# Performance work log

Hardware: AMD Instinct MI355X
Metric: run time of the kernel (lower is better)

Reference implementation:

```python
import jax, jax.numpy as jnp
import numpy as np

D_MODEL = 512
NHEAD = 8
HEAD_DIM = D_MODEL // NHEAD
WINDOW = 128


def setup_inputs() -> dict:
    key = jax.random.key(0)
    ks = jax.random.split(key, 5)
    B, S = 2, 2048
    scale = D_MODEL ** -0.5
    return {
        "x": jax.random.normal(ks[0], (B, S, D_MODEL), dtype=jnp.float32),
        # weights stored [in, out] so y = x @ W (equivalent to nn.Linear, bias=False)
        "Wq": jax.random.normal(ks[1], (D_MODEL, D_MODEL), dtype=jnp.float32) * scale,
        "Wk": jax.random.normal(ks[2], (D_MODEL, D_MODEL), dtype=jnp.float32) * scale,
        "Wv": jax.random.normal(ks[3], (D_MODEL, D_MODEL), dtype=jnp.float32) * scale,
        "Wo": jax.random.normal(ks[4], (D_MODEL, D_MODEL), dtype=jnp.float32) * scale,
    }


def reference(x, Wq, Wk, Wv, Wo):
    B, S, _ = x.shape
    # projections -> [B, H, S, D]
    def split_heads(y):
        return y.reshape(B, S, NHEAD, HEAD_DIM).transpose(0, 2, 1, 3)
    q = split_heads(x @ Wq)
    k = split_heads(x @ Wk)
    v = split_heads(x @ Wv)

    # causal sliding window: position p attends to [p - WINDOW + 1, p]
    pos = jnp.arange(S)
    offs = jnp.arange(WINDOW)
    idx = pos[:, None] - (WINDOW - 1) + offs[None, :]          # [S, W]
    valid = idx >= 0                                            # mask out-of-range (padded) slots
    idxc = jnp.clip(idx, 0, S - 1)

    k_w = k[:, :, idxc]                                         # [B, H, S, W, D]
    v_w = v[:, :, idxc]                                         # [B, H, S, W, D]

    inv_sqrt_d = jnp.float32(1.0 / np.sqrt(HEAD_DIM))
    scores = jnp.einsum('bhsd,bhswd->bhsw', q, k_w) * inv_sqrt_d
    scores = jnp.where(valid[None, None], scores, -jnp.inf)    # same as torch -inf masking of pads
    attn = jax.nn.softmax(scores, axis=-1)                      # last slot (self) always valid
    out = jnp.einsum('bhsw,bhswd->bhsd', attn, v_w)             # [B, H, S, D]
    out = out.transpose(0, 2, 1, 3).reshape(B, S, D_MODEL)
    return out @ Wo
```

## Files before the change

kernel.cpp:

```cpp
#include <hip/hip_runtime.h>

typedef __attribute__((ext_vector_type(8))) short bf16x8;
typedef __attribute__((ext_vector_type(4))) float f32x4;

#define D_MODEL 512
#define SEQ 2048
#define NB 2
#define NHEAD 8
#define HDIM 64
#define WIN 128

__device__ inline unsigned short f2bf(float f) {
    unsigned u = __float_as_uint(f);
    unsigned r = (u + 0x7fffu + ((u >> 16) & 1u)) >> 16;
    return (unsigned short)r;
}

__device__ inline void async_load16(const void* g, void* l) {
    __builtin_amdgcn_global_load_lds((const __attribute__((address_space(1))) void*)g,
                                     (__attribute__((address_space(3))) void*)l, 16, 0, 0);
}

__global__ __launch_bounds__(256) void conv_x(const float* __restrict__ x,
                                              unsigned short* __restrict__ xc) {
    int i = blockIdx.x * 256 + threadIdx.x;
    float4 v = ((const float4*)x)[i];
    ushort4 o;
    o.x = f2bf(v.x); o.y = f2bf(v.y); o.z = f2bf(v.z); o.w = f2bf(v.w);
    ((ushort4*)xc)[i] = o;
}

__global__ __launch_bounds__(256) void zero_out(float4* __restrict__ p) {
    p[blockIdx.x * 256 + threadIdx.x] = (float4){0.f, 0.f, 0.f, 0.f};
}

__global__ __launch_bounds__(256) void conv_wt(const float* __restrict__ Wq,
                                               const float* __restrict__ Wk,
                                               const float* __restrict__ Wv,
                                               const float* __restrict__ Wo,
                                               unsigned short* __restrict__ Wt) {
    __shared__ float tile[32 * 33];
    const int mat = blockIdx.z;
    const float* W = mat == 0 ? Wq : mat == 1 ? Wk : mat == 2 ? Wv : Wo;
    const int ti = blockIdx.x, tj = blockIdx.y;
    const int t = threadIdx.x;
    {
        int c = t & 31, r4 = (t >> 5) * 4;
        #pragma unroll
        for (int e = 0; e < 4; e++)
            tile[(r4 + e) * 33 + c] = W[(size_t)(ti * 32 + r4 + e) * 512 + tj * 32 + c];
    }
    __syncthreads();
    {
        int rr = t & 31, c4 = (t >> 5) * 4;
        #pragma unroll
        for (int e = 0; e < 4; e++)
            Wt[(size_t)mat * 262144 + (size_t)(tj * 32 + c4 + e) * 512 + ti * 32 + rr] =
                f2bf(tile[rr * 33 + c4 + e]);
    }
}

__device__ inline void storeC(float* C, size_t i, float v) { C[i] = v; }
__device__ inline void storeC(unsigned short* C, size_t i, float v) { C[i] = f2bf(v); }

template <typename OUT, bool ATOMIC>
__global__ __launch_bounds__(256) void gemm_bt(const unsigned short* __restrict__ A,
                                               const unsigned short* __restrict__ Bt,
                                               OUT* __restrict__ C, int Nstride,
                                               int kPerSplit) {
    __shared__ unsigned short As[128 * 32];
    __shared__ unsigned short Bs[128 * 32];
    const int t = threadIdx.x;
    const int w = t >> 6, l = t & 63;
    const int mBase = blockIdx.x * 128;
    const int nBase = blockIdx.y * 128;
    const int kBase = blockIdx.z * kPerSplit;
    const int r0 = t >> 2, koff = (t & 3) * 8;
    const unsigned short* a0 = A + (size_t)(mBase + r0) * 512 + koff;
    const unsigned short* a1 = A + (size_t)(mBase + 64 + r0) * 512 + koff;
    const unsigned short* b0 = Bt + (size_t)(nBase + r0) * 512 + koff;
    const unsigned short* b1 = Bt + (size_t)(nBase + 64 + r0) * 512 + koff;
    unsigned short* asd0 = &As[t * 8];
    unsigned short* asd1 = &As[2048 + t * 8];
    unsigned short* bsd0 = &Bs[t * 8];
    unsigned short* bsd1 = &Bs[2048 + t * 8];

    const int lane_m = l & 15;
    const int kg = (l >> 4) * 8;
    const int wr = (w >> 1) * 64, wc = (w & 1) * 64;

    f32x4 acc[4][4];
    #pragma unroll
    for (int i = 0; i < 4; i++)
        #pragma unroll
        for (int j = 0; j < 4; j++) acc[i][j] = (f32x4){0.f, 0.f, 0.f, 0.f};

    for (int k0 = kBase; k0 < kBase + kPerSplit; k0 += 32) {
        async_load16(a0 + k0, asd0);
        async_load16(a1 + k0, asd1);
        async_load16(b0 + k0, bsd0);
        async_load16(b1 + k0, bsd1);
        __syncthreads();
        bf16x8 af[4], bfr[4];
        #pragma unroll
        for (int i = 0; i < 4; i++)
            af[i] = *(const bf16x8*)&As[(wr + i * 16 + lane_m) * 32 + kg];
        #pragma unroll
        for (int j = 0; j < 4; j++)
            bfr[j] = *(const bf16x8*)&Bs[(wc + j * 16 + lane_m) * 32 + kg];
        #pragma unroll
        for (int i = 0; i < 4; i++)
            #pragma unroll
            for (int j = 0; j < 4; j++)
                acc[i][j] = __builtin_amdgcn_mfma_f32_16x16x32_bf16(af[i], bfr[j], acc[i][j], 0, 0, 0);
        __syncthreads();
    }
    const int rRow = (l >> 4) * 4;
    const int cCol = l & 15;
    #pragma unroll
    for (int i = 0; i < 4; i++)
        #pragma unroll
        for (int j = 0; j < 4; j++)
            #pragma unroll
            for (int r = 0; r < 4; r++) {
                size_t row = (size_t)(mBase + wr + i * 16 + rRow + r);
                size_t col = (size_t)(nBase + wc + j * 16 + cCol);
                if (ATOMIC)
                    unsafeAtomicAdd((float*)&C[row * (size_t)Nstride + col], acc[i][j][r]);
                else
                    storeC(C, row * (size_t)Nstride + col, acc[i][j][r]);
            }
}

__global__ __launch_bounds__(256) void transpose_v(const unsigned short* __restrict__ QKV,
                                                   unsigned short* __restrict__ Vtg) {
    __shared__ unsigned short tile[64 * 72];
    const int t = threadIdx.x;
    const int s0 = blockIdx.x * 64, h = blockIdx.y, b = blockIdx.z;
    const unsigned short* base = QKV + (size_t)b * SEQ * 1536 + 1024 + h * 64;
    for (int i = t; i < 64 * 8; i += 256) {
        int r = i >> 3, c8 = i & 7;
        *(uint4*)&tile[r * 72 + c8 * 8] = *(const uint4*)(base + (size_t)(s0 + r) * 1536 + c8 * 8);
    }
    __syncthreads();
    for (int i = t; i < 64 * 8; i += 256) {
        int d = i >> 3, c8 = i & 7;
        unsigned short tmp[8];
        #pragma unroll
        for (int e = 0; e < 8; e++) tmp[e] = tile[(c8 * 8 + e) * 72 + d];
        uint4 ov;
        ov.x = (unsigned)tmp[0] | ((unsigned)tmp[1] << 16);
        ov.y = (unsigned)tmp[2] | ((unsigned)tmp[3] << 16);
        ov.z = (unsigned)tmp[4] | ((unsigned)tmp[5] << 16);
        ov.w = (unsigned)tmp[6] | ((unsigned)tmp[7] << 16);
        *(uint4*)(Vtg + ((size_t)(b * 8 + h) * 64 + d) * SEQ + s0 + c8 * 8) = ov;
    }
}

__global__ __launch_bounds__(256) void attn_mfma(const unsigned short* __restrict__ QKV,
                                                 const unsigned short* __restrict__ Vtg,
                                                 unsigned short* __restrict__ AO) {
    __shared__ unsigned short Ks[192 * 72];
    __shared__ unsigned short Qs[64 * 72];
    __shared__ unsigned short Vs[64 * 200];
    __shared__ unsigned short Pb[4][16 * 40];

    const int t = threadIdx.x;
    const int w = t >> 6, l = t & 63;
    const int s0 = blockIdx.x * 64;
    const int h = blockIdx.y, b = blockIdx.z;
    const unsigned short* base = QKV + (size_t)b * SEQ * 1536;

    for (int i = t; i < 192 * 8; i += 256) {
        int j = i >> 3, c8 = i & 7;
        int g = s0 - 127 + j;
        g = g < 0 ? 0 : (g > SEQ - 1 ? SEQ - 1 : g);
        *(uint4*)&Ks[j * 72 + c8 * 8] =
            *(const uint4*)(base + (size_t)g * 1536 + 512 + h * 64 + c8 * 8);
    }
    for (int i = t; i < 64 * 8; i += 256) {
        int r = i >> 3, c8 = i & 7;
        *(uint4*)&Qs[r * 72 + c8 * 8] =
            *(const uint4*)(base + (size_t)(s0 + r) * 1536 + h * 64 + c8 * 8);
    }
    const unsigned short* vrow0 = Vtg + ((size_t)(b * 8 + h) * 64) * SEQ + (s0 - 127);
    for (int i = t; i < 64 * 24; i += 256) {
        int d = i / 24, c = i % 24;
        *(uint4*)&Vs[d * 200 + c * 8] = *(const uint4*)(vrow0 + (size_t)d * SEQ + c * 8);
    }
    __syncthreads();

    const int lm = l & 15, lk = (l >> 4) * 8;

    f32x4 sc[12];
    #pragma unroll
    for (int kb = 0; kb < 12; kb++) sc[kb] = (f32x4){0.f, 0.f, 0.f, 0.f};
    bf16x8 aq[2];
    #pragma unroll
    for (int ks = 0; ks < 2; ks++)
        aq[ks] = *(const bf16x8*)&Qs[(w * 16 + lm) * 72 + ks * 32 + lk];
    #pragma unroll
    for (int kb = 0; kb < 12; kb++) {
        #pragma unroll
        for (int ks = 0; ks < 2; ks++) {
            bf16x8 bk = *(const bf16x8*)&Ks[(kb * 16 + lm) * 72 + ks * 32 + lk];
            sc[kb] = __builtin_amdgcn_mfma_f32_16x16x32_bf16(aq[ks], bk, sc[kb], 0, 0, 0);
        }
    }

    const int qr0 = (l >> 4) * 4;
    const int jlo_g = 127 - s0;
    float mrow[4] = {-1e30f, -1e30f, -1e30f, -1e30f};
    #pragma unroll
    for (int kb = 0; kb < 12; kb++) {
        int j = kb * 16 + lm;
        #pragma unroll
        for (int r = 0; r < 4; r++) {
            int qi = w * 16 + qr0 + r;
            bool valid = (j >= qi) & (j <= qi + 127) & (j >= jlo_g);
            float v = valid ? sc[kb][r] * 0.125f : -1e30f;
            sc[kb][r] = v;
            mrow[r] = fmaxf(mrow[r], v);
        }
    }
    #pragma unroll
    for (int r = 0; r < 4; r++) {
        mrow[r] = fmaxf(mrow[r], __shfl_xor(mrow[r], 1));
        mrow[r] = fmaxf(mrow[r], __shfl_xor(mrow[r], 2));
        mrow[r] = fmaxf(mrow[r], __shfl_xor(mrow[r], 4));
        mrow[r] = fmaxf(mrow[r], __shfl_xor(mrow[r], 8));
    }
    float srow[4] = {0.f, 0.f, 0.f, 0.f};
    #pragma unroll
    for (int kb = 0; kb < 12; kb++)
        #pragma unroll
        for (int r = 0; r < 4; r++) {
            float p = __expf(sc[kb][r] - mrow[r]);
            sc[kb][r] = p;
            srow[r] += p;
        }
    #pragma unroll
    for (int r = 0; r < 4; r++) {
        srow[r] += __shfl_xor(srow[r], 1);
        srow[r] += __shfl_xor(srow[r], 2);
        srow[r] += __shfl_xor(srow[r], 4);
        srow[r] += __shfl_xor(srow[r], 8);
        srow[r] = 1.f / srow[r];
    }

    f32x4 ov[4];
    #pragma unroll
    for (int nb = 0; nb < 4; nb++) ov[nb] = (f32x4){0.f, 0.f, 0.f, 0.f};
    unsigned short* pb = &Pb[w][0];
    #pragma unroll
    for (int c = 0; c < 6; c++) {
        #pragma unroll
        for (int kk = 0; kk < 2; kk++)
            #pragma unroll
            for (int r = 0; r < 4; r++)
                pb[(qr0 + r) * 40 + kk * 16 + lm] = f2bf(sc[2 * c + kk][r]);
        bf16x8 ap = *(const bf16x8*)&pb[lm * 40 + lk];
        #pragma unroll
        for (int nb = 0; nb < 4; nb++) {
            bf16x8 bv = *(const bf16x8*)&Vs[(nb * 16 + lm) * 200 + c * 32 + lk];
            ov[nb] = __builtin_amdgcn_mfma_f32_16x16x32_bf16(ap, bv, ov[nb], 0, 0, 0);
        }
    }

    #pragma unroll
    for (int nb = 0; nb < 4; nb++)
        #pragma unroll
        for (int r = 0; r < 4; r++) {
            size_t row = (size_t)(b * SEQ + s0 + w * 16 + qr0 + r);
            AO[row * 512 + h * 64 + nb * 16 + lm] = f2bf(ov[nb][r] * srow[r]);
        }
}

extern "C" void kernel_launch(void* const* d_in, const int* in_sizes, int n_in,
                              void* d_out, int out_size, void* d_ws, size_t ws_size,
                              hipStream_t stream) {
    const float* x  = (const float*)d_in[0];
    const float* Wq = (const float*)d_in[1];
    const float* Wk = (const float*)d_in[2];
    const float* Wv = (const float*)d_in[3];
    const float* Wo = (const float*)d_in[4];
    float* out = (float*)d_out;

    char* ws = (char*)d_ws;
    unsigned short* xc  = (unsigned short*)ws;
    unsigned short* Wt  = (unsigned short*)(ws + 4u * 1024 * 1024);
    unsigned short* QKV = (unsigned short*)(ws + 6u * 1024 * 1024);
    unsigned short* AO  = (unsigned short*)(ws + 18u * 1024 * 1024);
    unsigned short* Vtg = (unsigned short*)(ws + 22u * 1024 * 1024 + 2048);

    conv_x<<<2048, 256, 0, stream>>>(x, xc);
    conv_wt<<<dim3(16, 16, 4), 256, 0, stream>>>(Wq, Wk, Wv, Wo, Wt);
    zero_out<<<2048, 256, 0, stream>>>((float4*)out);
    gemm_bt<unsigned short, false><<<dim3(32, 12, 1), 256, 0, stream>>>(xc, Wt, QKV, 1536, 512);
    transpose_v<<<dim3(32, 8, 2), 256, 0, stream>>>(QKV, Vtg);
    attn_mfma<<<dim3(32, 8, 2), 256, 0, stream>>>(QKV, Vtg, AO);
    gemm_bt<float, true><<<dim3(32, 4, 2), 256, 0, stream>>>(AO, Wt + 3 * 262144, out, 512, 256);
}
```

Baseline: 124.4 us.

## Cut launch count: merge prep kernels, fold V transpose into attention, drop split-K atomics

Merges the x and weight conversion kernels into one launch, removes the zero-fill and separate V-transpose kernels, and has the attention kernel transpose V into LDS itself using an XOR-swizzled layout. Both GEMMs now use 64-row tiles with full K per block and plain stores, so the output projection no longer needs atomics or a zeroed output. The aim is to cut launch overhead and extra global traffic on a launch-bound pipeline. In exchange, the GEMMs reuse less data per tile, and the scalar LDS transpose stores in attention may cause bank conflicts.

```diff
diff --git a/kernel.cpp b/kernel.cpp
--- a/kernel.cpp
+++ b/kernel.cpp
@@ -5,9 +5,7 @@
 
 #define D_MODEL 512
 #define SEQ 2048
-#define NB 2
 #define NHEAD 8
-#define HDIM 64
 #define WIN 128
 
 __device__ inline unsigned short f2bf(float f) {
@@ -21,29 +19,28 @@
                                      (__attribute__((address_space(3))) void*)l, 16, 0, 0);
 }
 
-__global__ __launch_bounds__(256) void conv_x(const float* __restrict__ x,
-                                              unsigned short* __restrict__ xc) {
-    int i = blockIdx.x * 256 + threadIdx.x;
-    float4 v = ((const float4*)x)[i];
-    ushort4 o;
-    o.x = f2bf(v.x); o.y = f2bf(v.y); o.z = f2bf(v.z); o.w = f2bf(v.w);
-    ((ushort4*)xc)[i] = o;
-}
-
-__global__ __launch_bounds__(256) void zero_out(float4* __restrict__ p) {
-    p[blockIdx.x * 256 + threadIdx.x] = (float4){0.f, 0.f, 0.f, 0.f};
-}
-
-__global__ __launch_bounds__(256) void conv_wt(const float* __restrict__ Wq,
-                                               const float* __restrict__ Wk,
-                                               const float* __restrict__ Wv,
-                                               const float* __restrict__ Wo,
-                                               unsigned short* __restrict__ Wt) {
+__global__ __launch_bounds__(256) void prep(const float* __restrict__ x,
+                                            const float* __restrict__ Wq,
+                                            const float* __restrict__ Wk,
+                                            const float* __restrict__ Wv,
+                                            const float* __restrict__ Wo,
+                                            unsigned short* __restrict__ xc,
+                                            unsigned short* __restrict__ Wt) {
     __shared__ float tile[32 * 33];
-    const int mat = blockIdx.z;
+    const int t = threadIdx.x;
+    if (blockIdx.x < 2048) {
+        int i = blockIdx.x * 256 + t;
+        float4 v = ((const float4*)x)[i];
+        ushort4 o;
+        o.x = f2bf(v.x); o.y = f2bf(v.y); o.z = f2bf(v.z); o.w = f2bf(v.w);
+        ((ushort4*)xc)[i] = o;
+        return;
+    }
+    int idx = blockIdx.x - 2048;
+    const int mat = idx >> 8;
+    const int rem = idx & 255;
+    const int ti = rem & 15, tj = rem >> 4;
     const float* W = mat == 0 ? Wq : mat == 1 ? Wk : mat == 2 ? Wv : Wo;
-    const int ti = blockIdx.x, tj = blockIdx.y;
-    const int t = threadIdx.x;
     {
         int c = t & 31, r4 = (t >> 5) * 4;
         #pragma unroll
@@ -63,102 +60,57 @@
 __device__ inline void storeC(float* C, size_t i, float v) { C[i] = v; }
 __device__ inline void storeC(unsigned short* C, size_t i, float v) { C[i] = f2bf(v); }
 
-template <typename OUT, bool ATOMIC>
-__global__ __launch_bounds__(256) void gemm_bt(const unsigned short* __restrict__ A,
-                                               const unsigned short* __restrict__ Bt,
-                                               OUT* __restrict__ C, int Nstride,
-                                               int kPerSplit) {
-    __shared__ unsigned short As[128 * 32];
-    __shared__ unsigned short Bs[128 * 32];
+template <typename OUT, int NT>
+__global__ __launch_bounds__(256) void gemm64(const unsigned short* __restrict__ A,
+                                              const unsigned short* __restrict__ Bt,
+                                              OUT* __restrict__ C, int Nstride) {
+    __shared__ unsigned short As[64 * 32];
+    __shared__ unsigned short Bs[NT * 16 * 32];
     const int t = threadIdx.x;
     const int w = t >> 6, l = t & 63;
-    const int mBase = blockIdx.x * 128;
-    const int nBase = blockIdx.y * 128;
-    const int kBase = blockIdx.z * kPerSplit;
+    const int mBase = blockIdx.x * 64;
+    const int nBase = blockIdx.y * (NT * 16);
     const int r0 = t >> 2, koff = (t & 3) * 8;
     const unsigned short* a0 = A + (size_t)(mBase + r0) * 512 + koff;
-    const unsigned short* a1 = A + (size_t)(mBase + 64 + r0) * 512 + koff;
     const unsigned short* b0 = Bt + (size_t)(nBase + r0) * 512 + koff;
     const unsigned short* b1 = Bt + (size_t)(nBase + 64 + r0) * 512 + koff;
-    unsigned short* asd0 = &As[t * 8];
-    unsigned short* asd1 = &As[2048 + t * 8];
+    unsigned short* asd  = &As[t * 8];
     unsigned short* bsd0 = &Bs[t * 8];
     unsigned short* bsd1 = &Bs[2048 + t * 8];
 
-    const int lane_m = l & 15;
+    const int lm = l & 15;
     const int kg = (l >> 4) * 8;
-    const int wr = (w >> 1) * 64, wc = (w & 1) * 64;
-
-    f32x4 acc[4][4];
-    #pragma unroll
-    for (int i = 0; i < 4; i++)
-        #pragma unroll
-        for (int j = 0; j < 4; j++) acc[i][j] = (f32x4){0.f, 0.f, 0.f, 0.f};
-
-    for (int k0 = kBase; k0 < kBase + kPerSplit; k0 += 32) {
-        async_load16(a0 + k0, asd0);
-        async_load16(a1 + k0, asd1);
+
+    f32x4 acc[NT];
+    #pragma unroll
+    for (int j = 0; j < NT; j++) acc[j] = (f32x4){0.f, 0.f, 0.f, 0.f};
+
+    for (int k0 = 0; k0 < 512; k0 += 32) {
+        async_load16(a0 + k0, asd);
         async_load16(b0 + k0, bsd0);
-        async_load16(b1 + k0, bsd1);
+        if (NT == 8) async_load16(b1 + k0, bsd1);
         __syncthreads();
-        bf16x8 af[4], bfr[4];
-        #pragma unroll
-        for (int i = 0; i < 4; i++)
-            af[i] = *(const bf16x8*)&As[(wr + i * 16 + lane_m) * 32 + kg];
-        #pragma unroll
-        for (int j = 0; j < 4; j++)
-            bfr[j] = *(const bf16x8*)&Bs[(wc + j * 16 + lane_m) * 32 + kg];
-        #pragma unroll
-        for (int i = 0; i < 4; i++)
-            #pragma unroll
-            for (int j = 0; j < 4; j++)
-                acc[i][j] = __builtin_amdgcn_mfma_f32_16x16x32_bf16(af[i], bfr[j], acc[i][j], 0, 0, 0);
+        bf16x8 af = *(const bf16x8*)&As[(w * 16 + lm) * 32 + kg];
+        #pragma unroll
+        for (int j = 0; j < NT; j++) {
+            bf16x8 bfr = *(const bf16x8*)&Bs[(j * 16 + lm) * 32 + kg];
+            acc[j] = __builtin_amdgcn_mfma_f32_16x16x32_bf16(af, bfr, acc[j], 0, 0, 0);
+        }
         __syncthreads();
     }
     const int rRow = (l >> 4) * 4;
     const int cCol = l & 15;
     #pragma unroll
-    for (int i = 0; i < 4; i++)
-        #pragma unroll
-        for (int j = 0; j < 4; j++)
-            #pragma unroll
-            for (int r = 0; r < 4; r++) {
-                size_t row = (size_t)(mBase + wr + i * 16 + rRow + r);
-                size_t col = (size_t)(nBase + wc + j * 16 + cCol);
-                if (ATOMIC)
-                    unsafeAtomicAdd((float*)&C[row * (size_t)Nstride + col], acc[i][j][r]);
-                else
-                    storeC(C, row * (size_t)Nstride + col, acc[i][j][r]);
-            }
-}
-
-__global__ __launch_bounds__(256) void transpose_v(const unsigned short* __restrict__ QKV,
-                                                   unsigned short* __restrict__ Vtg) {
-    __shared__ unsigned short tile[64 * 72];
-    const int t = threadIdx.x;
-    const int s0 = blockIdx.x * 64, h = blockIdx.y, b = blockIdx.z;
-    const unsigned short* base = QKV + (size_t)b * SEQ * 1536 + 1024 + h * 64;
-    for (int i = t; i < 64 * 8; i += 256) {
-        int r = i >> 3, c8 = i & 7;
-        *(uint4*)&tile[r * 72 + c8 * 8] = *(const uint4*)(base + (size_t)(s0 + r) * 1536 + c8 * 8);
-    }
-    __syncthreads();
-    for (int i = t; i < 64 * 8; i += 256) {
-        int d = i >> 3, c8 = i & 7;
-        unsigned short tmp[8];
-        #pragma unroll
-        for (int e = 0; e < 8; e++) tmp[e] = tile[(c8 * 8 + e) * 72 + d];
-        uint4 ov;
-        ov.x = (unsigned)tmp[0] | ((unsigned)tmp[1] << 16);
-        ov.y = (unsigned)tmp[2] | ((unsigned)tmp[3] << 16);
-        ov.z = (unsigned)tmp[4] | ((unsigned)tmp[5] << 16);
-        ov.w = (unsigned)tmp[6] | ((unsigned)tmp[7] << 16);
-        *(uint4*)(Vtg + ((size_t)(b * 8 + h) * 64 + d) * SEQ + s0 + c8 * 8) = ov;
-    }
+    for (int j = 0; j < NT; j++)
+        #pragma unroll
+        for (int r = 0; r < 4; r++) {
+            size_t row = (size_t)(mBase + w * 16 + rRow + r);
+            size_t col = (size_t)(nBase + j * 16 + cCol);
+            storeC(C, row * (size_t)Nstride + col, acc[j][r]);
+        }
 }
 
 __global__ __launch_bounds__(256) void attn_mfma(const unsigned short* __restrict__ QKV,
-                                                 const unsigned short* __restrict__ Vtg,
                                                  unsigned short* __restrict__ AO) {
     __shared__ unsigned short Ks[192 * 72];
     __shared__ unsigned short Qs[64 * 72];
@@ -183,10 +135,18 @@
         *(uint4*)&Qs[r * 72 + c8 * 8] =
             *(const uint4*)(base + (size_t)(s0 + r) * 1536 + h * 64 + c8 * 8);
     }
-    const unsigned short* vrow0 = Vtg + ((size_t)(b * 8 + h) * 64) * SEQ + (s0 - 127);
-    for (int i = t; i < 64 * 24; i += 256) {
-        int d = i / 24, c = i % 24;
-        *(uint4*)&Vs[d * 200 + c * 8] = *(const uint4*)(vrow0 + (size_t)d * SEQ + c * 8);
+    for (int i = t; i < 192 * 8; i += 256) {
+        int j = i >> 3, c8 = i & 7;
+        int g = s0 - 127 + j;
+        g = g < 0 ? 0 : (g > SEQ - 1 ? SEQ - 1 : g);
+        uint4 vv = *(const uint4*)(base + (size_t)g * 1536 + 1024 + h * 64 + c8 * 8);
+        unsigned short e16[8];
+        *(uint4*)e16 = vv;
+        int chunk = (j >> 3) ^ c8;
+        int off = chunk * 8 + (j & 7);
+        #pragma unroll
+        for (int e = 0; e < 8; e++)
+            Vs[(c8 * 8 + e) * 200 + off] = e16[e];
     }
     __syncthreads();
 
@@ -262,7 +222,10 @@
         bf16x8 ap = *(const bf16x8*)&pb[lm * 40 + lk];
         #pragma unroll
         for (int nb = 0; nb < 4; nb++) {
-            bf16x8 bv = *(const bf16x8*)&Vs[(nb * 16 + lm) * 200 + c * 32 + lk];
+            int d = nb * 16 + lm;
+            int cj = c * 4 + (l >> 4);
+            int off = ((cj ^ ((d >> 3) & 7)) * 8);
+            bf16x8 bv = *(const bf16x8*)&Vs[d * 200 + off];
             ov[nb] = __builtin_amdgcn_mfma_f32_16x16x32_bf16(ap, bv, ov[nb], 0, 0, 0);
         }
     }
@@ -291,13 +254,9 @@
     unsigned short* Wt  = (unsigned short*)(ws + 4u * 1024 * 1024);
     unsigned short* QKV = (unsigned short*)(ws + 6u * 1024 * 1024);
     unsigned short* AO  = (unsigned short*)(ws + 18u * 1024 * 1024);
-    unsigned short* Vtg = (unsigned short*)(ws + 22u * 1024 * 1024 + 2048);
-
-    conv_x<<<2048, 256, 0, stream>>>(x, xc);
-    conv_wt<<<dim3(16, 16, 4), 256, 0, stream>>>(Wq, Wk, Wv, Wo, Wt);
-    zero_out<<<2048, 256, 0, stream>>>((float4*)out);
-    gemm_bt<unsigned short, false><<<dim3(32, 12, 1), 256, 0, stream>>>(xc, Wt, QKV, 1536, 512);
-    transpose_v<<<dim3(32, 8, 2), 256, 0, stream>>>(QKV, Vtg);
-    attn_mfma<<<dim3(32, 8, 2), 256, 0, stream>>>(QKV, Vtg, AO);
-    gemm_bt<float, true><<<dim3(32, 4, 2), 256, 0, stream>>>(AO, Wt + 3 * 262144, out, 512, 256);
-}
+
+    prep<<<3072, 256, 0, stream>>>(x, Wq, Wk, Wv, Wo, xc, Wt);
+    gemm64<unsigned short, 8><<<dim3(64, 12), 256, 0, stream>>>(xc, Wt, QKV, 1536);
+    attn_mfma<<<dim3(32, 8, 2), 256, 0, stream>>>(QKV, AO);
+    gemm64<float, 4><<<dim3(64, 8), 256, 0, stream>>>(AO, Wt + 3 * 262144, out, 512);
+}
```

After: 104.4 us. -16.1%, faster.
